# Kernel optimization log

Measured on AMD Instinct MI355X. Metric: run time of the kernel, lower is better.

Reference implementation:

```python
import jax, jax.numpy as jnp
import numpy as np
import math

HEADS = 6
EPS = 1e-6


def _ln(x, a, b):
    # torch custom LayerNorm: unbiased std, divide by (std + eps)
    m = x.mean(axis=-1, keepdims=True)
    s = jnp.std(x, axis=-1, keepdims=True, ddof=1)
    return a * (x - m) / (s + EPS) + b


def _msa(z, wq, bq, wk, bk, wv, bv, wo, bo):
    B, S, D = z.shape
    dk = D // HEADS
    def proj(w, bias):
        return (z @ w.T + bias).reshape(B, S, HEADS, dk).transpose(0, 2, 1, 3)
    q = proj(wq, bq)  # [B,h,S,dk]
    k = proj(wk, bk)
    v = proj(wv, bv)
    scores = jnp.einsum('bhqd,bhkd->bhqk', q, k) / math.sqrt(dk)  # [B,h,S,S]
    p = jax.nn.softmax(scores, axis=-1)
    o = jnp.einsum('bhqk,bhkd->bhqd', p, v)
    o = o.transpose(0, 2, 1, 3).reshape(B, S, D)
    return o @ wo.T + bo


def setup_inputs() -> dict:
    key = jax.random.key(0)
    ks = jax.random.split(key, 6)
    B, S, D = 2, 4096, 384
    sc = 0.02
    return {
        'x': jax.random.normal(ks[0], (B, S, D), dtype=jnp.float32),
        'a0': jnp.ones((D,), jnp.float32), 'b0': jnp.zeros((D,), jnp.float32),
        'ra0': jnp.ones((D,), jnp.float32), 'rb0': jnp.zeros((D,), jnp.float32),
        'ra1': jnp.ones((D,), jnp.float32), 'rb1': jnp.zeros((D,), jnp.float32),
        'wq': jax.random.normal(ks[1], (D, D), jnp.float32) * sc, 'bq': jnp.zeros((D,), jnp.float32),
        'wk': jax.random.normal(ks[2], (D, D), jnp.float32) * sc, 'bk': jnp.zeros((D,), jnp.float32),
        'wv': jax.random.normal(ks[3], (D, D), jnp.float32) * sc, 'bv': jnp.zeros((D,), jnp.float32),
        'wo': jax.random.normal(ks[4], (D, D), jnp.float32) * sc, 'bo': jnp.zeros((D,), jnp.float32),
    }


def reference(x, a0, b0, ra0, rb0, ra1, rb1, wq, bq, wk, bk, wv, bv, wo, bo):
    # Faithful to source: both residual connections invoke MSA (MLP is never
    # called in the original forward), and the input to MSA is LayerNorm'd
    # twice (residual_conn norm, then norm[0]). Dropout = 0 (eval).
    z = _ln(_ln(x, ra0, rb0), a0, b0)
    x = x + _msa(z, wq, bq, wk, bk, wv, bv, wo, bo)
    z = _ln(_ln(x, ra1, rb1), a0, b0)
    x = x + _msa(z, wq, bq, wk, bk, wv, bv, wo, bo)
    return x
```

## Files before the change

kernel.cpp:

```cpp
#include <hip/hip_runtime.h>
#include <hip/hip_bf16.h>
#include <math.h>

typedef __bf16 bf16;
typedef __bf16 bf16x4 __attribute__((ext_vector_type(4)));
typedef __bf16 bf16x8 __attribute__((ext_vector_type(8)));
typedef float  f32x4  __attribute__((ext_vector_type(4)));

#define SEQ 4096
#define DM  384
#define NH  6
#define DK  64
#define NB  2
#define WN  (DM * DM)
#define EPSLN 1e-6f

__device__ __forceinline__ float ldT(const void* p, size_t i, int f32) {
    return f32 ? ((const float*)p)[i] : (float)(((const bf16*)p)[i]);
}

__global__ __launch_bounds__(256) void ln2_kernel(
    const void* __restrict__ x, int xf32,
    const float* __restrict__ ra, const float* __restrict__ rb,
    const float* __restrict__ a0, const float* __restrict__ b0, bf16* __restrict__ z)
{
    int row  = blockIdx.x * 4 + (threadIdx.x >> 6);
    int lane = threadIdx.x & 63;
    size_t base = (size_t)row * DM;

    float v[6];
    float s = 0.f;
    #pragma unroll
    for (int i = 0; i < 6; i++) { v[i] = ldT(x, base + lane + i * 64, xf32); s += v[i]; }
    #pragma unroll
    for (int off = 1; off < 64; off <<= 1) s += __shfl_xor(s, off);
    float m = s * (1.f / DM);
    float sq = 0.f;
    #pragma unroll
    for (int i = 0; i < 6; i++) { float d = v[i] - m; sq += d * d; }
    #pragma unroll
    for (int off = 1; off < 64; off <<= 1) sq += __shfl_xor(sq, off);
    float inv = 1.f / (sqrtf(sq * (1.f / (DM - 1))) + EPSLN);

    s = 0.f;
    #pragma unroll
    for (int i = 0; i < 6; i++) {
        int c = lane + i * 64;
        v[i] = ra[c] * (v[i] - m) * inv + rb[c];
        s += v[i];
    }
    #pragma unroll
    for (int off = 1; off < 64; off <<= 1) s += __shfl_xor(s, off);
    m = s * (1.f / DM);
    sq = 0.f;
    #pragma unroll
    for (int i = 0; i < 6; i++) { float d = v[i] - m; sq += d * d; }
    #pragma unroll
    for (int off = 1; off < 64; off <<= 1) sq += __shfl_xor(sq, off);
    inv = 1.f / (sqrtf(sq * (1.f / (DM - 1))) + EPSLN);

    bf16* zr = z + base;
    #pragma unroll
    for (int i = 0; i < 6; i++) {
        int c = lane + i * 64;
        zr[c] = (bf16)(a0[c] * (v[i] - m) * inv + b0[c]);
    }
}

__global__ __launch_bounds__(256) void qkv_kernel(
    const bf16* __restrict__ A,
    const float* __restrict__ wq, const float* __restrict__ wk, const float* __restrict__ wv,
    const float* __restrict__ bq, const float* __restrict__ bk, const float* __restrict__ bv,
    bf16* __restrict__ qkout, bf16* __restrict__ vt)
{
    const int z = blockIdx.z;
    const float* W    = (z == 0) ? wq : (z == 1) ? wk : wv;
    const float* bias = (z == 0) ? bq : (z == 1) ? bk : bv;

    const int t = threadIdx.x;
    const int wave = t >> 6, lane = t & 63;
    const int l15 = lane & 15, quad = lane >> 4;
    const int wr = wave >> 1, wc = wave & 1;
    const int m0 = blockIdx.x * 128;
    const int n0 = blockIdx.y * 64;

    __shared__ __attribute__((aligned(16))) bf16 As[128][72];
    __shared__ __attribute__((aligned(16))) bf16 Bs[64][72];

    const int r0 = t >> 2;
    const int c0 = (t & 3) * 16;

    const bf16*  aptr0 = A + (size_t)(m0 + r0) * DM + c0;
    const bf16*  aptr1 = A + (size_t)(m0 + 64 + r0) * DM + c0;
    const float* bptr  = W + (size_t)(n0 + r0) * DM + c0;

    bf16x8 ra00 = *(const bf16x8*)(aptr0);
    bf16x8 ra01 = *(const bf16x8*)(aptr0 + 8);
    bf16x8 ra10 = *(const bf16x8*)(aptr1);
    bf16x8 ra11 = *(const bf16x8*)(aptr1 + 8);
    f32x4 wv0 = *(const f32x4*)(bptr);
    f32x4 wv1 = *(const f32x4*)(bptr + 4);
    f32x4 wv2 = *(const f32x4*)(bptr + 8);
    f32x4 wv3 = *(const f32x4*)(bptr + 12);

    f32x4 acc[4][2];
    #pragma unroll
    for (int mi = 0; mi < 4; mi++)
        #pragma unroll
        for (int ni = 0; ni < 2; ni++) acc[mi][ni] = (f32x4){0.f, 0.f, 0.f, 0.f};

    for (int kk = 0; kk < DM; kk += 64) {
        __syncthreads();
        *(bf16x8*)&As[r0][c0]          = ra00;
        *(bf16x8*)&As[r0][c0 + 8]      = ra01;
        *(bf16x8*)&As[64 + r0][c0]     = ra10;
        *(bf16x8*)&As[64 + r0][c0 + 8] = ra11;
        {
            bf16x8 b0v, b1v;
            #pragma unroll
            for (int j = 0; j < 4; j++) {
                b0v[j] = (bf16)wv0[j]; b0v[4 + j] = (bf16)wv1[j];
                b1v[j] = (bf16)wv2[j]; b1v[4 + j] = (bf16)wv3[j];
            }
            *(bf16x8*)&Bs[r0][c0]     = b0v;
            *(bf16x8*)&Bs[r0][c0 + 8] = b1v;
        }
        __syncthreads();
        if (kk + 64 < DM) {
            ra00 = *(const bf16x8*)(aptr0 + kk + 64);
            ra01 = *(const bf16x8*)(aptr0 + kk + 64 + 8);
            ra10 = *(const bf16x8*)(aptr1 + kk + 64);
            ra11 = *(const bf16x8*)(aptr1 + kk + 64 + 8);
            wv0 = *(const f32x4*)(bptr + kk + 64);
            wv1 = *(const f32x4*)(bptr + kk + 64 + 4);
            wv2 = *(const f32x4*)(bptr + kk + 64 + 8);
            wv3 = *(const f32x4*)(bptr + kk + 64 + 12);
        }

        #pragma unroll
        for (int kc = 0; kc < 64; kc += 32) {
            bf16x8 af[4], bf[2];
            #pragma unroll
            for (int mi = 0; mi < 4; mi++)
                af[mi] = *(const bf16x8*)&As[wr * 64 + mi * 16 + l15][kc + quad * 8];
            #pragma unroll
            for (int ni = 0; ni < 2; ni++)
                bf[ni] = *(const bf16x8*)&Bs[wc * 32 + ni * 16 + l15][kc + quad * 8];
            #pragma unroll
            for (int mi = 0; mi < 4; mi++)
                #pragma unroll
                for (int ni = 0; ni < 2; ni++)
                    acc[mi][ni] = __builtin_amdgcn_mfma_f32_16x16x32_bf16(af[mi], bf[ni], acc[mi][ni], 0, 0, 0);
        }
    }

    if (z < 2) {
        bf16* out = qkout + (size_t)z * ((size_t)NB * SEQ * DM);
        #pragma unroll
        for (int ni = 0; ni < 2; ni++) {
            int col = n0 + wc * 32 + ni * 16 + l15;
            float bb = bias[col];
            #pragma unroll
            for (int mi = 0; mi < 4; mi++) {
                #pragma unroll
                for (int r = 0; r < 4; r++) {
                    int row = m0 + wr * 64 + mi * 16 + quad * 4 + r;
                    out[(size_t)row * DM + col] = (bf16)(acc[mi][ni][r] + bb);
                }
            }
        }
    } else {
        #pragma unroll
        for (int ni = 0; ni < 2; ni++) {
            int col = n0 + wc * 32 + ni * 16 + l15;
            int h = col >> 6, d = col & 63;
            float bb = bias[col];
            #pragma unroll
            for (int mi = 0; mi < 4; mi++) {
                int row0 = m0 + wr * 64 + mi * 16 + quad * 4;
                int b = row0 >> 12, s0 = row0 & (SEQ - 1);
                bf16x4 ov;
                #pragma unroll
                for (int r = 0; r < 4; r++) ov[r] = (bf16)(acc[mi][ni][r] + bb);
                *(bf16x4*)(vt + (((size_t)b * NH + h) * DK + d) * SEQ + s0) = ov;
            }
        }
    }
}

__device__ __forceinline__ bf16x8 combineA(
    const bf16* __restrict__ o0, const bf16* __restrict__ o1,
    const float* __restrict__ lsum, int row, int kcol)
{
    int b = row >> 12, s = row & (SEQ - 1);
    int h = kcol >> 6;
    size_t lidx = ((size_t)b * NH + h) * SEQ + s;
    float inv = 1.f / (lsum[lidx] + lsum[(size_t)(NB * NH * SEQ) + lidx]);
    size_t idx = (size_t)row * DM + kcol;
    bf16x8 a = *(const bf16x8*)(o0 + idx);
    bf16x8 c = *(const bf16x8*)(o1 + idx);
    bf16x8 r;
    #pragma unroll
    for (int j = 0; j < 8; j++) r[j] = (bf16)(((float)a[j] + (float)c[j]) * inv);
    return r;
}

__global__ __launch_bounds__(256) void proj_kernel(
    const bf16* __restrict__ o0, const bf16* __restrict__ o1,
    const float* __restrict__ lsum,
    const float* __restrict__ wo, const float* __restrict__ bo,
    const void* __restrict__ xin, int f32in,
    void* __restrict__ xout, int f32out)
{
    const int t = threadIdx.x;
    const int wave = t >> 6, lane = t & 63;
    const int l15 = lane & 15, quad = lane >> 4;
    const int wr = wave >> 1, wc = wave & 1;
    const int m0 = blockIdx.x * 64;
    const int n0 = blockIdx.y * 64;

    __shared__ __attribute__((aligned(16))) bf16 As[64][72];
    __shared__ __attribute__((aligned(16))) bf16 Bs[64][72];

    const int r0 = t >> 2;
    const int c0 = (t & 3) * 16;
    const int arow = m0 + r0;
    const float* bptr = wo + (size_t)(n0 + r0) * DM + c0;

    bf16x8 ca0 = combineA(o0, o1, lsum, arow, c0);
    bf16x8 ca1 = combineA(o0, o1, lsum, arow, c0 + 8);
    f32x4 wv0 = *(const f32x4*)(bptr);
    f32x4 wv1 = *(const f32x4*)(bptr + 4);
    f32x4 wv2 = *(const f32x4*)(bptr + 8);
    f32x4 wv3 = *(const f32x4*)(bptr + 12);

    f32x4 acc[2][2];
    #pragma unroll
    for (int mi = 0; mi < 2; mi++)
        #pragma unroll
        for (int ni = 0; ni < 2; ni++) acc[mi][ni] = (f32x4){0.f, 0.f, 0.f, 0.f};

    for (int kk = 0; kk < DM; kk += 64) {
        __syncthreads();
        *(bf16x8*)&As[r0][c0]     = ca0;
        *(bf16x8*)&As[r0][c0 + 8] = ca1;
        {
            bf16x8 b0v, b1v;
            #pragma unroll
            for (int j = 0; j < 4; j++) {
                b0v[j] = (bf16)wv0[j]; b0v[4 + j] = (bf16)wv1[j];
                b1v[j] = (bf16)wv2[j]; b1v[4 + j] = (bf16)wv3[j];
            }
            *(bf16x8*)&Bs[r0][c0]     = b0v;
            *(bf16x8*)&Bs[r0][c0 + 8] = b1v;
        }
        __syncthreads();
        if (kk + 64 < DM) {
            ca0 = combineA(o0, o1, lsum, arow, kk + 64 + c0);
            ca1 = combineA(o0, o1, lsum, arow, kk + 64 + c0 + 8);
            wv0 = *(const f32x4*)(bptr + kk + 64);
            wv1 = *(const f32x4*)(bptr + kk + 64 + 4);
            wv2 = *(const f32x4*)(bptr + kk + 64 + 8);
            wv3 = *(const f32x4*)(bptr + kk + 64 + 12);
        }

        #pragma unroll
        for (int kc = 0; kc < 64; kc += 32) {
            bf16x8 af[2], bf[2];
            #pragma unroll
            for (int mi = 0; mi < 2; mi++)
                af[mi] = *(const bf16x8*)&As[wr * 32 + mi * 16 + l15][kc + quad * 8];
            #pragma unroll
            for (int ni = 0; ni < 2; ni++)
                bf[ni] = *(const bf16x8*)&Bs[wc * 32 + ni * 16 + l15][kc + quad * 8];
            #pragma unroll
            for (int mi = 0; mi < 2; mi++)
                #pragma unroll
                for (int ni = 0; ni < 2; ni++)
                    acc[mi][ni] = __builtin_amdgcn_mfma_f32_16x16x32_bf16(af[mi], bf[ni], acc[mi][ni], 0, 0, 0);
        }
    }

    #pragma unroll
    for (int ni = 0; ni < 2; ni++) {
        int col = n0 + wc * 32 + ni * 16 + l15;
        float bb = bo[col];
        #pragma unroll
        for (int mi = 0; mi < 2; mi++) {
            #pragma unroll
            for (int r = 0; r < 4; r++) {
                size_t idx = (size_t)(m0 + wr * 32 + mi * 16 + quad * 4 + r) * DM + col;
                float val = ldT(xin, idx, f32in) + acc[mi][ni][r] + bb;
                if (f32out) ((float*)xout)[idx] = val;
                else        ((bf16*)xout)[idx] = (bf16)val;
            }
        }
    }
}

__global__ __launch_bounds__(256, 3) void attn_kernel(
    const bf16* __restrict__ q, const bf16* __restrict__ k, const bf16* __restrict__ vt,
    bf16* __restrict__ o0, bf16* __restrict__ o1, float* __restrict__ lsum)
{
    int qt = blockIdx.x, h = blockIdx.y;
    int b = blockIdx.z >> 1, split = blockIdx.z & 1;
    int wave = threadIdx.x >> 6, lane = threadIdx.x & 63;
    int l15 = lane & 15, quad = lane >> 4;
    int q0 = qt * 128;
    const int kvbase = split * (SEQ / 2);
    size_t basebh = (size_t)b * SEQ * DM + (size_t)h * DK;

    __shared__ __attribute__((aligned(16))) bf16 KsP0[128][72];
    __shared__ __attribute__((aligned(16))) bf16 Vt[64][136];
    __shared__ __attribute__((aligned(16))) bf16 P1[4][16][136];
    bf16 (*P0)[16][136] = (bf16 (*)[16][136])&KsP0[0][0];

    bf16x8 aq[2][2];
    #pragma unroll
    for (int qg = 0; qg < 2; qg++) {
        const bf16* qp = q + basebh + (size_t)(q0 + qg * 64 + wave * 16 + l15) * DM + quad * 8;
        aq[qg][0] = *(const bf16x8*)(qp);
        aq[qg][1] = *(const bf16x8*)(qp + 32);
    }

    const float c2 = 0.18033688011112042f;
    float lr[2][2] = {{0.f, 0.f}, {0.f, 0.f}};
    f32x4 oacc[2][4];
    #pragma unroll
    for (int qg = 0; qg < 2; qg++)
        #pragma unroll
        for (int mt = 0; mt < 4; mt++) oacc[qg][mt] = (f32x4){0.f, 0.f, 0.f, 0.f};

    const int sd  = threadIdx.x >> 2;
    const int sk0 = (threadIdx.x & 3) * 32;
    const bf16* vtrow0 = vt + (((size_t)b * NH + h) * DK + sd) * SEQ + sk0;
    const int skk = threadIdx.x >> 1;
    const int sdk = (threadIdx.x & 1) * 32;
    const bf16* krow0 = k + basebh + (size_t)skk * DM + sdk;

    bf16x8 vr0 = *(const bf16x8*)(vtrow0 + kvbase);
    bf16x8 vr1 = *(const bf16x8*)(vtrow0 + kvbase + 8);
    bf16x8 vr2 = *(const bf16x8*)(vtrow0 + kvbase + 16);
    bf16x8 vr3 = *(const bf16x8*)(vtrow0 + kvbase + 24);
    bf16x8 kr0 = *(const bf16x8*)(krow0 + (size_t)kvbase * DM);
    bf16x8 kr1 = *(const bf16x8*)(krow0 + (size_t)kvbase * DM + 8);
    bf16x8 kr2 = *(const bf16x8*)(krow0 + (size_t)kvbase * DM + 16);
    bf16x8 kr3 = *(const bf16x8*)(krow0 + (size_t)kvbase * DM + 24);

    for (int it = 0; it < 16; it++) {
        __syncthreads();
        *(bf16x8*)&Vt[sd][sk0]      = vr0;
        *(bf16x8*)&Vt[sd][sk0 + 8]  = vr1;
        *(bf16x8*)&Vt[sd][sk0 + 16] = vr2;
        *(bf16x8*)&Vt[sd][sk0 + 24] = vr3;
        *(bf16x8*)&KsP0[skk][sdk]      = kr0;
        *(bf16x8*)&KsP0[skk][sdk + 8]  = kr1;
        *(bf16x8*)&KsP0[skk][sdk + 16] = kr2;
        *(bf16x8*)&KsP0[skk][sdk + 24] = kr3;
        __syncthreads();

        {
            int kvn = (it + 1 < 16) ? kvbase + (it + 1) * 128 : kvbase;
            const bf16* vp = vtrow0 + kvn;
            vr0 = *(const bf16x8*)(vp);
            vr1 = *(const bf16x8*)(vp + 8);
            vr2 = *(const bf16x8*)(vp + 16);
            vr3 = *(const bf16x8*)(vp + 24);
            const bf16* kp2 = krow0 + (size_t)kvn * DM;
            kr0 = *(const bf16x8*)(kp2);
            kr1 = *(const bf16x8*)(kp2 + 8);
            kr2 = *(const bf16x8*)(kp2 + 16);
            kr3 = *(const bf16x8*)(kp2 + 24);
        }

        bf16x4 pk0[8];
        #pragma unroll
        for (int g = 0; g < 8; g++) {
            bf16x8 kf0 = *(const bf16x8*)&KsP0[g * 16 + l15][quad * 8];
            bf16x8 kf1 = *(const bf16x8*)&KsP0[g * 16 + l15][quad * 8 + 32];
            f32x4 s0 = (f32x4){0.f, 0.f, 0.f, 0.f};
            f32x4 s1 = (f32x4){0.f, 0.f, 0.f, 0.f};
            s0 = __builtin_amdgcn_mfma_f32_16x16x32_bf16(kf0, aq[0][0], s0, 0, 0, 0);
            s1 = __builtin_amdgcn_mfma_f32_16x16x32_bf16(kf0, aq[1][0], s1, 0, 0, 0);
            s0 = __builtin_amdgcn_mfma_f32_16x16x32_bf16(kf1, aq[0][1], s0, 0, 0, 0);
            s1 = __builtin_amdgcn_mfma_f32_16x16x32_bf16(kf1, aq[1][1], s1, 0, 0, 0);
            bf16x4 t1;
            #pragma unroll
            for (int r = 0; r < 4; r++) {
                float p0 = __builtin_amdgcn_exp2f(s0[r] * c2);
                float p1 = __builtin_amdgcn_exp2f(s1[r] * c2);
                lr[0][r & 1] += p0;
                lr[1][r & 1] += p1;
                pk0[g][r] = (bf16)p0;
                t1[r] = (bf16)p1;
            }
            *(bf16x4*)&P1[wave][l15][g * 16 + quad * 4] = t1;
        }

        __syncthreads();

        #pragma unroll
        for (int g = 0; g < 8; g++)
            *(bf16x4*)&P0[wave][l15][g * 16 + quad * 4] = pk0[g];

        #pragma unroll
        for (int c = 0; c < 4; c++) {
            bf16x8 bp0 = *(const bf16x8*)(&P0[wave][l15][c * 32 + quad * 8]);
            bf16x8 bp1 = *(const bf16x8*)(&P1[wave][l15][c * 32 + quad * 8]);
            #pragma unroll
            for (int mt = 0; mt < 4; mt++) {
                bf16x8 av = *(const bf16x8*)(&Vt[mt * 16 + l15][c * 32 + quad * 8]);
                oacc[0][mt] = __builtin_amdgcn_mfma_f32_16x16x32_bf16(av, bp0, oacc[0][mt], 0, 0, 0);
                oacc[1][mt] = __builtin_amdgcn_mfma_f32_16x16x32_bf16(av, bp1, oacc[1][mt], 0, 0, 0);
            }
        }
    }

    bf16* osel = split ? o1 : o0;
    #pragma unroll
    for (int qg = 0; qg < 2; qg++) {
        float lrun = lr[qg][0] + lr[qg][1];
        lrun += __shfl_xor(lrun, 16);
        lrun += __shfl_xor(lrun, 32);
        int row = q0 + qg * 64 + wave * 16 + l15;
        bf16* op = osel + basebh + (size_t)row * DM + quad * 4;
        #pragma unroll
        for (int mt = 0; mt < 4; mt++) {
            bf16x4 ov;
            #pragma unroll
            for (int r = 0; r < 4; r++) ov[r] = (bf16)oacc[qg][mt][r];
            *(bf16x4*)(op + mt * 16) = ov;
        }
        if (quad == 0)
            lsum[(size_t)split * (NB * NH * SEQ) + ((size_t)b * NH + h) * SEQ + row] = lrun;
    }
}

extern "C" void kernel_launch(void* const* d_in, const int* in_sizes, int n_in,
                              void* d_out, int out_size, void* d_ws, size_t ws_size,
                              hipStream_t stream) {
    const size_t SZ = (size_t)NB * SEQ * DM;

    const float* x   = (const float*)d_in[0];
    const float* a0  = (const float*)d_in[1];
    const float* b0  = (const float*)d_in[2];
    const float* ra0 = (const float*)d_in[3];
    const float* rb0 = (const float*)d_in[4];
    const float* ra1 = (const float*)d_in[5];
    const float* rb1 = (const float*)d_in[6];
    const float* wq  = (const float*)d_in[7];  const float* bq = (const float*)d_in[8];
    const float* wk  = (const float*)d_in[9];  const float* bk = (const float*)d_in[10];
    const float* wv  = (const float*)d_in[11]; const float* bv = (const float*)d_in[12];
    const float* wo  = (const float*)d_in[13]; const float* bo = (const float*)d_in[14];

    bf16* zob = (bf16*)d_ws;
    bf16* qb  = zob + SZ;
    bf16* kb  = qb + SZ;
    bf16* vtb = kb + SZ;
    bf16* x1  = vtb + SZ;
    bf16* o1b = x1 + SZ;
    float* lsum = (float*)(o1b + SZ);

    dim3 gLN(NB * SEQ / 4);
    dim3 gG(NB * SEQ / 128, DM / 64, 3);
    dim3 gP(NB * SEQ / 64, DM / 64);
    dim3 gA(SEQ / 128, NH, NB * 2);

    ln2_kernel<<<gLN, 256, 0, stream>>>(x, 1, ra0, rb0, a0, b0, zob);
    qkv_kernel<<<gG, 256, 0, stream>>>(zob, wq, wk, wv, bq, bk, bv, qb, vtb);
    attn_kernel<<<gA, 256, 0, stream>>>(qb, kb, vtb, zob, o1b, lsum);
    proj_kernel<<<gP, 256, 0, stream>>>(zob, o1b, lsum, wo, bo, x, 1, x1, 0);
    ln2_kernel<<<gLN, 256, 0, stream>>>(x1, 0, ra1, rb1, a0, b0, zob);
    qkv_kernel<<<gG, 256, 0, stream>>>(zob, wq, wk, wv, bq, bk, bv, qb, vtb);
    attn_kernel<<<gA, 256, 0, stream>>>(qb, kb, vtb, zob, o1b, lsum);
    proj_kernel<<<gP, 256, 0, stream>>>(zob, o1b, lsum, wo, bo, x1, 0, d_out, 1);
}
```

Measured before the change: 311.4 us.

## Switch attention to 32x32x16 MFMA with register-resident P via permlane swap

Rewrites the attention inner loop to use 32x32x16 bf16 MFMA tiles instead of 16x16x32. The softmax probabilities stay in registers and are rearranged with a permlane32 swap (or a shuffle fallback) into the B-operand layout, so the P round-trip through shared memory and the extra barrier are gone. The V tile in shared memory uses a new padded layout split by KV chunk. This should cut LDS traffic and synchronisation, but it changes the accumulator register footprint, which may affect occupancy under the 3-block launch bound.

```diff
diff --git a/kernel.cpp b/kernel.cpp
--- a/kernel.cpp
+++ b/kernel.cpp
@@ -3,9 +3,13 @@
 #include <math.h>
 
 typedef __bf16 bf16;
+typedef __bf16 bf16x2 __attribute__((ext_vector_type(2)));
 typedef __bf16 bf16x4 __attribute__((ext_vector_type(4)));
 typedef __bf16 bf16x8 __attribute__((ext_vector_type(8)));
 typedef float  f32x4  __attribute__((ext_vector_type(4)));
+typedef float  f32x16 __attribute__((ext_vector_type(16)));
+typedef int    i32x2  __attribute__((ext_vector_type(2)));
+typedef int    i32x4  __attribute__((ext_vector_type(4)));
 
 #define SEQ 4096
 #define DM  384
@@ -298,44 +302,65 @@
     }
 }
 
+__device__ __forceinline__ unsigned packbf(float lo, float hi) {
+    bf16x2 t;
+    t[0] = (bf16)lo;
+    t[1] = (bf16)hi;
+    return __builtin_bit_cast(unsigned, t);
+}
+
+__device__ __forceinline__ i32x2 halfswap(unsigned a, unsigned b) {
+#if defined(__has_builtin) && __has_builtin(__builtin_amdgcn_permlane32_swap)
+    return __builtin_amdgcn_permlane32_swap((int)a, (int)b, false, false);
+#else
+    int pa = __shfl_xor((int)a, 32);
+    int pb = __shfl_xor((int)b, 32);
+    bool hi = (threadIdx.x & 32) != 0;
+    i32x2 r;
+    r[0] = hi ? pb : (int)a;
+    r[1] = hi ? (int)b : pa;
+    return r;
+#endif
+}
+
+#define V_RS 40
+#define V_TS 2576
+
 __global__ __launch_bounds__(256, 3) void attn_kernel(
     const bf16* __restrict__ q, const bf16* __restrict__ k, const bf16* __restrict__ vt,
     bf16* __restrict__ o0, bf16* __restrict__ o1, float* __restrict__ lsum)
 {
     int qt = blockIdx.x, h = blockIdx.y;
     int b = blockIdx.z >> 1, split = blockIdx.z & 1;
-    int wave = threadIdx.x >> 6, lane = threadIdx.x & 63;
-    int l15 = lane & 15, quad = lane >> 4;
-    int q0 = qt * 128;
+    const int t = threadIdx.x;
+    const int wave = t >> 6, lane = t & 63;
+    const int L = lane & 31, hf = lane >> 5;
+    const int q0 = qt * 128;
     const int kvbase = split * (SEQ / 2);
     size_t basebh = (size_t)b * SEQ * DM + (size_t)h * DK;
 
-    __shared__ __attribute__((aligned(16))) bf16 KsP0[128][72];
-    __shared__ __attribute__((aligned(16))) bf16 Vt[64][136];
-    __shared__ __attribute__((aligned(16))) bf16 P1[4][16][136];
-    bf16 (*P0)[16][136] = (bf16 (*)[16][136])&KsP0[0][0];
-
-    bf16x8 aq[2][2];
-    #pragma unroll
-    for (int qg = 0; qg < 2; qg++) {
-        const bf16* qp = q + basebh + (size_t)(q0 + qg * 64 + wave * 16 + l15) * DM + quad * 8;
-        aq[qg][0] = *(const bf16x8*)(qp);
-        aq[qg][1] = *(const bf16x8*)(qp + 32);
-    }
+    __shared__ __attribute__((aligned(16))) bf16 Ks[128][72];
+    __shared__ __attribute__((aligned(16))) bf16 VtL[4 * V_TS];
+
+    const int qrow = q0 + wave * 32 + L;
+    const bf16* qp = q + basebh + (size_t)qrow * DM + 8 * hf;
+    bf16x8 aq[4];
+    #pragma unroll
+    for (int ks = 0; ks < 4; ks++) aq[ks] = *(const bf16x8*)(qp + 16 * ks);
 
     const float c2 = 0.18033688011112042f;
-    float lr[2][2] = {{0.f, 0.f}, {0.f, 0.f}};
-    f32x4 oacc[2][4];
-    #pragma unroll
-    for (int qg = 0; qg < 2; qg++)
-        #pragma unroll
-        for (int mt = 0; mt < 4; mt++) oacc[qg][mt] = (f32x4){0.f, 0.f, 0.f, 0.f};
-
-    const int sd  = threadIdx.x >> 2;
-    const int sk0 = (threadIdx.x & 3) * 32;
-    const bf16* vtrow0 = vt + (((size_t)b * NH + h) * DK + sd) * SEQ + sk0;
-    const int skk = threadIdx.x >> 1;
-    const int sdk = (threadIdx.x & 1) * 32;
+    float lrA = 0.f, lrB = 0.f;
+    f32x16 oacc[2];
+    #pragma unroll
+    for (int db = 0; db < 2; db++)
+        #pragma unroll
+        for (int r = 0; r < 16; r++) oacc[db][r] = 0.f;
+
+    const int sd  = t >> 2;
+    const int sc  = t & 3;
+    const bf16* vtrow0 = vt + (((size_t)b * NH + h) * DK + sd) * SEQ + sc * 32;
+    const int skk = t >> 1;
+    const int sdk = (t & 1) * 32;
     const bf16* krow0 = k + basebh + (size_t)skk * DM + sdk;
 
     bf16x8 vr0 = *(const bf16x8*)(vtrow0 + kvbase);
@@ -349,14 +374,17 @@
 
     for (int it = 0; it < 16; it++) {
         __syncthreads();
-        *(bf16x8*)&Vt[sd][sk0]      = vr0;
-        *(bf16x8*)&Vt[sd][sk0 + 8]  = vr1;
-        *(bf16x8*)&Vt[sd][sk0 + 16] = vr2;
-        *(bf16x8*)&Vt[sd][sk0 + 24] = vr3;
-        *(bf16x8*)&KsP0[skk][sdk]      = kr0;
-        *(bf16x8*)&KsP0[skk][sdk + 8]  = kr1;
-        *(bf16x8*)&KsP0[skk][sdk + 16] = kr2;
-        *(bf16x8*)&KsP0[skk][sdk + 24] = kr3;
+        {
+            bf16* vw = &VtL[sc * V_TS + sd * V_RS];
+            *(bf16x8*)(vw)      = vr0;
+            *(bf16x8*)(vw + 8)  = vr1;
+            *(bf16x8*)(vw + 16) = vr2;
+            *(bf16x8*)(vw + 24) = vr3;
+            *(bf16x8*)&Ks[skk][sdk]      = kr0;
+            *(bf16x8*)&Ks[skk][sdk + 8]  = kr1;
+            *(bf16x8*)&Ks[skk][sdk + 16] = kr2;
+            *(bf16x8*)&Ks[skk][sdk + 24] = kr3;
+        }
         __syncthreads();
 
         {
@@ -373,67 +401,64 @@
             kr3 = *(const bf16x8*)(kp2 + 24);
         }
 
-        bf16x4 pk0[8];
-        #pragma unroll
-        for (int g = 0; g < 8; g++) {
-            bf16x8 kf0 = *(const bf16x8*)&KsP0[g * 16 + l15][quad * 8];
-            bf16x8 kf1 = *(const bf16x8*)&KsP0[g * 16 + l15][quad * 8 + 32];
-            f32x4 s0 = (f32x4){0.f, 0.f, 0.f, 0.f};
-            f32x4 s1 = (f32x4){0.f, 0.f, 0.f, 0.f};
-            s0 = __builtin_amdgcn_mfma_f32_16x16x32_bf16(kf0, aq[0][0], s0, 0, 0, 0);
-            s1 = __builtin_amdgcn_mfma_f32_16x16x32_bf16(kf0, aq[1][0], s1, 0, 0, 0);
-            s0 = __builtin_amdgcn_mfma_f32_16x16x32_bf16(kf1, aq[0][1], s0, 0, 0, 0);
-            s1 = __builtin_amdgcn_mfma_f32_16x16x32_bf16(kf1, aq[1][1], s1, 0, 0, 0);
-            bf16x4 t1;
-            #pragma unroll
-            for (int r = 0; r < 4; r++) {
-                float p0 = __builtin_amdgcn_exp2f(s0[r] * c2);
-                float p1 = __builtin_amdgcn_exp2f(s1[r] * c2);
-                lr[0][r & 1] += p0;
-                lr[1][r & 1] += p1;
-                pk0[g][r] = (bf16)p0;
-                t1[r] = (bf16)p1;
-            }
-            *(bf16x4*)&P1[wave][l15][g * 16 + quad * 4] = t1;
-        }
-
-        __syncthreads();
-
-        #pragma unroll
-        for (int g = 0; g < 8; g++)
-            *(bf16x4*)&P0[wave][l15][g * 16 + quad * 4] = pk0[g];
-
-        #pragma unroll
-        for (int c = 0; c < 4; c++) {
-            bf16x8 bp0 = *(const bf16x8*)(&P0[wave][l15][c * 32 + quad * 8]);
-            bf16x8 bp1 = *(const bf16x8*)(&P1[wave][l15][c * 32 + quad * 8]);
-            #pragma unroll
-            for (int mt = 0; mt < 4; mt++) {
-                bf16x8 av = *(const bf16x8*)(&Vt[mt * 16 + l15][c * 32 + quad * 8]);
-                oacc[0][mt] = __builtin_amdgcn_mfma_f32_16x16x32_bf16(av, bp0, oacc[0][mt], 0, 0, 0);
-                oacc[1][mt] = __builtin_amdgcn_mfma_f32_16x16x32_bf16(av, bp1, oacc[1][mt], 0, 0, 0);
+        #pragma unroll
+        for (int kvb = 0; kvb < 4; kvb++) {
+            f32x16 sacc;
+            #pragma unroll
+            for (int r = 0; r < 16; r++) sacc[r] = 0.f;
+            #pragma unroll
+            for (int ks = 0; ks < 4; ks++) {
+                bf16x8 kf = *(const bf16x8*)&Ks[kvb * 32 + L][ks * 16 + hf * 8];
+                sacc = __builtin_amdgcn_mfma_f32_32x32x16_bf16(kf, aq[ks], sacc, 0, 0, 0);
+            }
+
+            float p[16];
+            #pragma unroll
+            for (int r = 0; r < 16; r++) {
+                p[r] = __builtin_amdgcn_exp2f(sacc[r] * c2);
+                if (r & 1) lrB += p[r]; else lrA += p[r];
+            }
+
+            unsigned pk0[4], pk1[4];
+            #pragma unroll
+            for (int R = 0; R < 4; R++) {
+                pk0[R] = packbf(p[4 * R], p[4 * R + 1]);
+                pk1[R] = packbf(p[4 * R + 2], p[4 * R + 3]);
+            }
+
+            #pragma unroll
+            for (int c2i = 0; c2i < 2; c2i++) {
+                i32x2 r0 = halfswap(pk0[2 * c2i], pk0[2 * c2i + 1]);
+                i32x2 r1 = halfswap(pk1[2 * c2i], pk1[2 * c2i + 1]);
+                i32x4 w;
+                w[0] = r0[0]; w[1] = r1[0]; w[2] = r0[1]; w[3] = r1[1];
+                bf16x8 pb = __builtin_bit_cast(bf16x8, w);
+                #pragma unroll
+                for (int db = 0; db < 2; db++) {
+                    bf16x8 av = *(const bf16x8*)&VtL[kvb * V_TS + (db * 32 + L) * V_RS
+                                                     + c2i * 16 + hf * 8];
+                    oacc[db] = __builtin_amdgcn_mfma_f32_32x32x16_bf16(av, pb, oacc[db], 0, 0, 0);
+                }
             }
         }
     }
 
     bf16* osel = split ? o1 : o0;
-    #pragma unroll
-    for (int qg = 0; qg < 2; qg++) {
-        float lrun = lr[qg][0] + lr[qg][1];
-        lrun += __shfl_xor(lrun, 16);
-        lrun += __shfl_xor(lrun, 32);
-        int row = q0 + qg * 64 + wave * 16 + l15;
-        bf16* op = osel + basebh + (size_t)row * DM + quad * 4;
-        #pragma unroll
-        for (int mt = 0; mt < 4; mt++) {
+    float lrow = lrA + lrB;
+    lrow += __shfl_xor(lrow, 32);
+    bf16* op = osel + basebh + (size_t)qrow * DM;
+    #pragma unroll
+    for (int db = 0; db < 2; db++) {
+        #pragma unroll
+        for (int R = 0; R < 4; R++) {
             bf16x4 ov;
             #pragma unroll
-            for (int r = 0; r < 4; r++) ov[r] = (bf16)oacc[qg][mt][r];
-            *(bf16x4*)(op + mt * 16) = ov;
-        }
-        if (quad == 0)
-            lsum[(size_t)split * (NB * NH * SEQ) + ((size_t)b * NH + h) * SEQ + row] = lrun;
-    }
+            for (int r = 0; r < 4; r++) ov[r] = (bf16)oacc[db][4 * R + r];
+            *(bf16x4*)(op + db * 32 + R * 8 + hf * 4) = ov;
+        }
+    }
+    if (hf == 0)
+        lsum[(size_t)split * (NB * NH * SEQ) + ((size_t)b * NH + h) * SEQ + qrow] = lrow;
 }
 
 extern "C" void kernel_launch(void* const* d_in, const int* in_sizes, int n_in,
```

Measured after the change: 294.0 us. 5.6% less time.
